# Optimization experiments

Hardware: AMD Instinct MI355X
Metric: run time of the kernel (lower is better)

## Reference

```python
import math
import jax, jax.numpy as jnp
import numpy as np

D_MODEL = 1024
NHEAD = 16
HEAD_DIM = D_MODEL // NHEAD
BATCH = 2
SEQ = 2048


def setup_inputs() -> dict:
    key = jax.random.key(0)
    ks = jax.random.split(key, 8)
    data = jax.random.normal(ks[0], (BATCH, SEQ, D_MODEL), dtype=jnp.float32)
    temporal = jax.random.uniform(ks[1], (BATCH, SEQ), dtype=jnp.float32)
    mask = jnp.zeros((SEQ, SEQ), dtype=jnp.float32)
    s = 1.0 / math.sqrt(D_MODEL)
    Wq = jax.random.normal(ks[2], (D_MODEL, D_MODEL), dtype=jnp.float32) * s
    Wk = jax.random.normal(ks[3], (D_MODEL, D_MODEL), dtype=jnp.float32) * s
    Wv = jax.random.normal(ks[4], (D_MODEL, D_MODEL), dtype=jnp.float32) * s
    bq = jax.random.normal(ks[5], (D_MODEL,), dtype=jnp.float32) * 0.02
    bk = jax.random.normal(ks[6], (D_MODEL,), dtype=jnp.float32) * 0.02
    bv = jax.random.normal(ks[7], (D_MODEL,), dtype=jnp.float32) * 0.02
    return {"data": data, "temporal": temporal, "mask": mask,
            "Wq": Wq, "bq": bq, "Wk": Wk, "bk": bk, "Wv": Wv, "bv": bv}


def _rotate_half_pairs(x):
    # x: [..., s] with s even; pairs (x0,x1) -> (-x1, x0) interleaved
    x2 = x.reshape(x.shape[:-1] + (-1, 2))  # [..., s//2, 2]
    rot = jnp.stack([-x2[..., 1], x2[..., 0]], axis=-1)
    return rot.reshape(x.shape)


def reference(data, temporal, mask, Wq, bq, Wk, bk, Wv, bv):
    B, L, D = data.shape
    H, S = NHEAD, HEAD_DIM
    scale = math.sqrt(S)

    query = (data @ Wq + bq).reshape(B, L, H, S)
    key_ = (data @ Wk + bk).reshape(B, L, H, S)
    value = (data @ Wv + bv).reshape(B, L, H, S)

    # freq = 10000^(-arange(0, S, 2)/S), repeat_interleave(2) -> [S]
    freq = jnp.power(10000.0, -jnp.arange(0, S, 2, dtype=jnp.float32) / S)
    freq = jnp.repeat(freq, 2)
    freqs = temporal[:, :, None] * freq[None, None, :]  # [B, L, S]
    cosine = jnp.cos(freqs)[:, :, None, :]  # [B, L, 1, S]
    sine = jnp.sin(freqs)[:, :, None, :]

    rq = query * cosine + _rotate_half_pairs(query) * sine
    rk = key_ * cosine + _rotate_half_pairs(key_) * sine

    logits = jnp.einsum('bqhs,bkhs->bhqk', rq, rk) / scale
    logits = logits + mask  # mask: [L, L], broadcasts over b,h
    weights = jax.nn.softmax(logits, axis=-1)
    context = jnp.einsum('bhqk,bkhs->bqhs', weights, value)
    return context.reshape(B, L, D)
```

## Files before the change

kernel.cpp:

```cpp
#include <hip/hip_runtime.h>
#include <hip/hip_bf16.h>

#define D_MODEL 1024
#define NHEAD   16
#define HEAD_DIM 64
#define BATCH   2
#define SEQ     2048
#define NTOK    (BATCH*SEQ)

#define FREQ_LOG2 0.20762050593046015f

typedef short  bfrag __attribute__((ext_vector_type(8)));
typedef float  ffrag __attribute__((ext_vector_type(4)));

__device__ inline ushort f2bf(float x) {
    __hip_bfloat16 h = __float2bfloat16(x);
    return __builtin_bit_cast(ushort, h);
}
__device__ inline float bf2f(ushort u) {
    return __builtin_bit_cast(float, (uint)u << 16);
}
__device__ inline void split_bf(float x, ushort& hi, ushort& lo) {
    __hip_bfloat16 h = __float2bfloat16(x);
    hi = __builtin_bit_cast(ushort, h);
    lo = f2bf(x - __bfloat162float(h));
}

__device__ inline void gload16(const ushort* g, ushort* l) {
    __builtin_amdgcn_global_load_lds(
        (const __attribute__((address_space(1))) void*)g,
        (__attribute__((address_space(3))) void*)l, 16, 0, 0);
}

__device__ inline void barrier_lds_only() {
    asm volatile("s_waitcnt lgkmcnt(0)\n\ts_barrier" ::: "memory");
}

__global__ __launch_bounds__(256)
void prep(const float* __restrict__ data, ushort* __restrict__ Ahi,
          ushort* __restrict__ Alo,
          const float* __restrict__ mask, ushort* __restrict__ Mbf,
          int* __restrict__ MZnz,
          const float* __restrict__ Wq, const float* __restrict__ Wk,
          const float* __restrict__ Wv, ushort* __restrict__ WThi)
{
    __shared__ float T[64][65];
    __shared__ int bnz;
    const int bid = blockIdx.x, t = threadIdx.x;

    if (bid < 4096) {
        const int i4 = (bid * 256 + t) * 4;
        const float4 v = *(const float4*)(data + i4);
        ushort4 h, l;
        split_bf(v.x, h.x, l.x); split_bf(v.y, h.y, l.y);
        split_bf(v.z, h.z, l.z); split_bf(v.w, h.w, l.w);
        *(ushort4*)(Ahi + i4) = h;
        *(ushort4*)(Alo + i4) = l;
        return;
    }
    if (bid < 8192) {
        const int mi = bid - 4096;
        const int i4 = (mi * 256 + t) * 4;
        const float4 v = *(const float4*)(mask + i4);
        ushort4 h;
        h.x = f2bf(v.x); h.y = f2bf(v.y); h.z = f2bf(v.z); h.w = f2bf(v.w);
        *(ushort4*)(Mbf + i4) = h;
        const int nz = (v.x != 0.f) || (v.y != 0.f) || (v.z != 0.f) || (v.w != 0.f);
        if (t == 0) bnz = 0;
        __syncthreads();
        if (nz) atomicOr(&bnz, 1);
        __syncthreads();
        if (t == 0) MZnz[mi] = bnz;
        return;
    }
    const int id  = bid - 8192;
    const int z   = id >> 8;
    const int rem = id & 255;
    const int k0  = (rem & 15) * 64, n0 = (rem >> 4) * 64;
    const float* W = (z == 0) ? Wq : (z == 1) ? Wk : Wv;
    ushort* thi = WThi + (size_t)z * D_MODEL * D_MODEL;

    #pragma unroll
    for (int i = 0; i < 4; i++) {
        const int f = i * 256 + t, r = f >> 4, c = (f & 15) * 4;
        const float4 v = *(const float4*)(W + (size_t)(k0 + r) * D_MODEL + n0 + c);
        T[r][c] = v.x; T[r][c + 1] = v.y; T[r][c + 2] = v.z; T[r][c + 3] = v.w;
    }
    __syncthreads();
    #pragma unroll
    for (int i = 0; i < 4; i++) {
        const int f = i * 256 + t, nr = f >> 4, kc = (f & 15) * 4;
        ushort4 h;
        h.x = f2bf(T[kc + 0][nr]);
        h.y = f2bf(T[kc + 1][nr]);
        h.z = f2bf(T[kc + 2][nr]);
        h.w = f2bf(T[kc + 3][nr]);
        const size_t o = (size_t)(n0 + nr) * D_MODEL + k0 + kc;
        *(ushort4*)(thi + o) = h;
    }
}

#define BK 32

union GemmSM {
    ushort st[2][3][128 * BK];
    float  c[64 * 132];
};

__global__ __launch_bounds__(256, 3)
void gemm_qkv(const ushort* __restrict__ Ahi, const ushort* __restrict__ Alo,
              const ushort* __restrict__ WThi,
              const float* __restrict__ bq, const float* __restrict__ bk,
              const float* __restrict__ bv, const float* __restrict__ temporal,
              const int* __restrict__ MZnz, int* __restrict__ Flag,
              ushort* __restrict__ Qhi, ushort* __restrict__ Qlo,
              ushort* __restrict__ Khi,
              ushort* __restrict__ VT)
{
    __shared__ GemmSM sm;
    __shared__ int flg;
    const int bidl = blockIdx.x;
    const int xcd  = bidl & 7, kk = bidl >> 3;
    const int m0   = (xcd * 4 + (kk & 3)) * 128;
    const int nz   = kk >> 2;
    const int n0   = (nz & 7) * 128;
    const int z    = nz >> 3;

    const int t = threadIdx.x;

    if (bidl == 0) {
        if (t == 0) flg = 0;
        __syncthreads();
        int acc = 0;
        const int4* z4 = (const int4*)MZnz;
        #pragma unroll
        for (int i = 0; i < 4; i++) {
            const int4 v = z4[t * 4 + i];
            acc |= v.x | v.y | v.z | v.w;
        }
        if (acc) atomicOr(&flg, 1);
        __syncthreads();
        if (t == 0) Flag[0] = flg;
    }

    const float* bias = (z == 0) ? bq : (z == 1) ? bk : bv;
    const ushort* Bh = WThi + (size_t)z * D_MODEL * D_MODEL;

    const int w = t >> 6, lane = t & 63;
    const int lane15 = lane & 15, quad8 = (lane >> 4) * 8, quad = lane >> 4;
    const int wm = (w >> 1) * 64, wn = (w & 1) * 64;

    ffrag acc[4][4];
    #pragma unroll
    for (int i = 0; i < 4; i++)
        #pragma unroll
        for (int j = 0; j < 4; j++) acc[i][j] = (ffrag){0.f, 0.f, 0.f, 0.f};

    const int wr = w * 32;
    const int lr = lane >> 2;
    const int lc = (((lane & 3) ^ ((lane >> 3) & 3))) * 8;

    auto stage = [&](int bsel, int k0) {
        #pragma unroll
        for (int ch = 0; ch < 2; ch++) {
            const int rb = wr + ch * 16;
            const ushort* ga = Ahi + (size_t)(m0 + rb + lr) * D_MODEL + k0 + lc;
            const ushort* gl = Alo + (size_t)(m0 + rb + lr) * D_MODEL + k0 + lc;
            const ushort* gb = Bh  + (size_t)(n0 + rb + lr) * D_MODEL + k0 + lc;
            gload16(ga, &sm.st[bsel][0][rb * BK]);
            gload16(gl, &sm.st[bsel][1][rb * BK]);
            gload16(gb, &sm.st[bsel][2][rb * BK]);
        }
    };

    stage(0, 0);
    __syncthreads();

    const int rdsw = (quad ^ ((lane15 >> 1) & 3)) * 8;

    int buf = 0;
    for (int k0 = 0; k0 < D_MODEL; k0 += BK) {
        if (k0 + BK < D_MODEL) stage(buf ^ 1, k0 + BK);

        bfrag ah[4], al[4];
        #pragma unroll
        for (int mt = 0; mt < 4; mt++) {
            ah[mt] = *(const bfrag*)&sm.st[buf][0][(wm + mt * 16 + lane15) * BK + rdsw];
            al[mt] = *(const bfrag*)&sm.st[buf][1][(wm + mt * 16 + lane15) * BK + rdsw];
        }
        #pragma unroll
        for (int nt = 0; nt < 4; nt++) {
            const bfrag bh = *(const bfrag*)&sm.st[buf][2][(wn + nt * 16 + lane15) * BK + rdsw];
            #pragma unroll
            for (int mt = 0; mt < 4; mt++) {
                ffrag a = acc[mt][nt];
                a = __builtin_amdgcn_mfma_f32_16x16x32_bf16(ah[mt], bh, a, 0, 0, 0);
                a = __builtin_amdgcn_mfma_f32_16x16x32_bf16(al[mt], bh, a, 0, 0, 0);
                acc[mt][nt] = a;
            }
        }
        __syncthreads();
        buf ^= 1;
    }

    float bn[4];
    #pragma unroll
    for (int nt = 0; nt < 4; nt++) bn[nt] = bias[n0 + wn + nt * 16 + lane15];

    const int CST = (z == 2) ? 129 : 132;

    #pragma unroll
    for (int p = 0; p < 2; p++) {
        if (p) __syncthreads();
        if ((w >> 1) == p) {
            #pragma unroll
            for (int mt = 0; mt < 4; mt++)
                #pragma unroll
                for (int nt = 0; nt < 4; nt++)
                    #pragma unroll
                    for (int rr = 0; rr < 4; rr++)
                        sm.c[(mt * 16 + quad * 4 + rr) * CST + wn + nt * 16 + lane15] =
                            acc[mt][nt][rr] + bn[nt];
        }
        __syncthreads();

        if (z < 2) {
            ushort* ohi = (z == 0) ? Qhi : Khi;
            const float sc = (z == 0) ? 0.125f : 1.0f;
            #pragma unroll
            for (int i = 0; i < 8; i++) {
                const int f = i * 256 + t, r = f >> 5, c4 = (f & 31) * 4;
                float4 v = *(float4*)&sm.c[r * 132 + c4];
                const int m = m0 + p * 64 + r;
                const float tv = temporal[m];
                const float fr0 = exp2f(-(float)(c4 & 63) * FREQ_LOG2);
                const float fr1 = exp2f(-(float)((c4 + 2) & 63) * FREQ_LOG2);
                float s0, c0, s1, c1v;
                __sincosf(tv * fr0, &s0, &c0);
                __sincosf(tv * fr1, &s1, &c1v);
                const float y0 = (v.x * c0 - v.y * s0) * sc;
                const float y1 = (v.y * c0 + v.x * s0) * sc;
                const float y2 = (v.z * c1v - v.w * s1) * sc;
                const float y3 = (v.w * c1v + v.z * s1) * sc;
                ushort4 h, l;
                split_bf(y0, h.x, l.x); split_bf(y1, h.y, l.y);
                split_bf(y2, h.z, l.z); split_bf(y3, h.w, l.w);
                const size_t o = (size_t)m * D_MODEL + n0 + c4;
                *(ushort4*)(ohi + o) = h;
                if (z == 0) *(ushort4*)(Qlo + o) = l;
            }
        } else {
            const int bb = m0 >> 11;
            #pragma unroll
            for (int i = 0; i < 4; i++) {
                const int cid = i * 256 + t, col = cid >> 3, tg = (cid & 7) * 8;
                ushort u8[8];
                #pragma unroll
                for (int j = 0; j < 8; j++) u8[j] = f2bf(sm.c[(tg + j) * 129 + col]);
                const int ncol = n0 + col, hh = ncol >> 6, d = ncol & 63;
                const size_t dst = ((size_t)(bb * NHEAD + hh) * HEAD_DIM + d) * SEQ +
                                   (m0 & (SEQ - 1)) + p * 64 + tg;
                *(int4*)(VT + dst) = *(int4*)u8;
            }
        }
    }
}

__global__ __launch_bounds__(256, 2)
void attn_mfma(const ushort* __restrict__ Qhi, const ushort* __restrict__ Qlo,
               const ushort* __restrict__ Khi,
               const ushort* __restrict__ VT,  const ushort* __restrict__ maskbf,
               const int* __restrict__ Flag,
               float* __restrict__ out)
{
    __shared__ ushort lsK[2][64 * 64], lsV[2][64 * 64], lsP[128 * 64];

    const int bid  = blockIdx.x;
    const int bh   = (bid & 7) * 4 + (bid >> 7);
    const int qb   = (bid >> 3) & 15;
    const int b    = bh >> 4, h = bh & 15;
    const int q0   = qb * 128;

    const int t = threadIdx.x, w = t >> 6, lane = t & 63;
    const int lane15 = lane & 15, quad = lane >> 4;
    const size_t tok0 = (size_t)b * SEQ;

    const int mz = Flag[0];

    bfrag qh[2][2], ql[2][2];
    #pragma unroll
    for (int su = 0; su < 2; su++) {
        const size_t qrow = (tok0 + q0 + w * 32 + su * 16 + lane15) * D_MODEL +
                            h * HEAD_DIM;
        #pragma unroll
        for (int ks = 0; ks < 2; ks++) {
            qh[su][ks] = *(const bfrag*)(Qhi + qrow + ks * 32 + quad * 8);
            ql[su][ks] = *(const bfrag*)(Qlo + qrow + ks * 32 + quad * 8);
        }
    }

    ffrag of[2][4];
    float l_i[2][4];
    #pragma unroll
    for (int su = 0; su < 2; su++)
        #pragma unroll
        for (int nt = 0; nt < 4; nt++) {
            of[su][nt] = (ffrag){0.f, 0.f, 0.f, 0.f};
            l_i[su][nt] = 0.f;
        }

    const int r1 = t >> 3,  c1 = (t & 7) * 8;
    const int sw = ((t & 7) ^ (r1 & 7)) * 8;
    const ushort* Kh0 = Khi + tok0 * D_MODEL + h * HEAD_DIM;
    const ushort* Vt0 = VT + (size_t)(b * NHEAD + h) * HEAD_DIM * SEQ;

    int4 pk0 = *(const int4*)(Kh0 + (size_t)r1 * D_MODEL + c1);
    int4 pk1 = *(const int4*)(Kh0 + (size_t)(32 + r1) * D_MODEL + c1);
    int4 pv0 = *(const int4*)(Vt0 + (size_t)r1 * SEQ + c1);
    int4 pv1 = *(const int4*)(Vt0 + (size_t)(32 + r1) * SEQ + c1);

    *(int4*)&lsK[0][r1 * 64 + sw]        = pk0;
    *(int4*)&lsK[0][(32 + r1) * 64 + sw] = pk1;
    *(int4*)&lsV[0][r1 * 64 + sw]        = pv0;
    *(int4*)&lsV[0][(32 + r1) * 64 + sw] = pv1;

    pk0 = *(const int4*)(Kh0 + (size_t)(64 + r1) * D_MODEL + c1);
    pk1 = *(const int4*)(Kh0 + (size_t)(96 + r1) * D_MODEL + c1);
    pv0 = *(const int4*)(Vt0 + (size_t)r1 * SEQ + 64 + c1);
    pv1 = *(const int4*)(Vt0 + (size_t)(32 + r1) * SEQ + 64 + c1);
    barrier_lds_only();

    const ushort* mrow0 = maskbf + (size_t)(q0 + w * 32 + quad * 4) * SEQ;
    const ushort* mrow1 = maskbf + (size_t)(q0 + w * 32 + 16 + quad * 4) * SEQ;

    const int krd  = lane15 & 7;
    const int keyr = (((lane15 >> 2) & 3) << 1) | (lane15 & 1);

    int cur = 0;
    for (int kt = 0; kt < SEQ; kt += 64) {
        if (kt + 64 < SEQ) {
            *(int4*)&lsK[cur ^ 1][r1 * 64 + sw]        = pk0;
            *(int4*)&lsK[cur ^ 1][(32 + r1) * 64 + sw] = pk1;
            *(int4*)&lsV[cur ^ 1][r1 * 64 + sw]        = pv0;
            *(int4*)&lsV[cur ^ 1][(32 + r1) * 64 + sw] = pv1;
        }

        float mv0[4][4], mv1[4][4];
        if (mz) {
            #pragma unroll
            for (int nt = 0; nt < 4; nt++)
                #pragma unroll
                for (int rr = 0; rr < 4; rr++) {
                    mv0[nt][rr] = bf2f(mrow0[(size_t)rr * SEQ + kt + nt * 16 + lane15]);
                    mv1[nt][rr] = bf2f(mrow1[(size_t)rr * SEQ + kt + nt * 16 + lane15]);
                }
        }

        const int ktn = (kt + 128 < SEQ) ? kt + 128 : 0;
        pk0 = *(const int4*)(Kh0 + (size_t)(ktn + r1) * D_MODEL + c1);
        pk1 = *(const int4*)(Kh0 + (size_t)(ktn + 32 + r1) * D_MODEL + c1);
        pv0 = *(const int4*)(Vt0 + (size_t)r1 * SEQ + ktn + c1);
        pv1 = *(const int4*)(Vt0 + (size_t)(32 + r1) * SEQ + ktn + c1);

        ffrag s0[4], s1[4];
        __builtin_amdgcn_s_setprio(1);
        #pragma unroll
        for (int nt = 0; nt < 4; nt++) {
            const bfrag kf0 = *(const bfrag*)&lsK[cur][(nt * 16 + lane15) * 64 +
                                                       ((0 + quad) ^ krd) * 8];
            const bfrag kf1 = *(const bfrag*)&lsK[cur][(nt * 16 + lane15) * 64 +
                                                       ((4 + quad) ^ krd) * 8];
            ffrag a0 = (ffrag){0.f, 0.f, 0.f, 0.f};
            ffrag a1 = (ffrag){0.f, 0.f, 0.f, 0.f};
            a0 = __builtin_amdgcn_mfma_f32_16x16x32_bf16(qh[0][0], kf0, a0, 0, 0, 0);
            a0 = __builtin_amdgcn_mfma_f32_16x16x32_bf16(ql[0][0], kf0, a0, 0, 0, 0);
            a0 = __builtin_amdgcn_mfma_f32_16x16x32_bf16(qh[0][1], kf1, a0, 0, 0, 0);
            a0 = __builtin_amdgcn_mfma_f32_16x16x32_bf16(ql[0][1], kf1, a0, 0, 0, 0);
            a1 = __builtin_amdgcn_mfma_f32_16x16x32_bf16(qh[1][0], kf0, a1, 0, 0, 0);
            a1 = __builtin_amdgcn_mfma_f32_16x16x32_bf16(ql[1][0], kf0, a1, 0, 0, 0);
            a1 = __builtin_amdgcn_mfma_f32_16x16x32_bf16(qh[1][1], kf1, a1, 0, 0, 0);
            a1 = __builtin_amdgcn_mfma_f32_16x16x32_bf16(ql[1][1], kf1, a1, 0, 0, 0);
            s0[nt] = a0;
            s1[nt] = a1;
        }
        __builtin_amdgcn_s_setprio(0);

        #pragma unroll
        for (int nt = 0; nt < 4; nt++)
            #pragma unroll
            for (int rr = 0; rr < 4; rr++) {
                const int pchk = (2 * nt + (lane15 >> 3)) ^ ((quad << 1) | (rr & 1));
                float x0 = s0[nt][rr];
                float x1 = s1[nt][rr];
                if (mz) { x0 += mv0[nt][rr]; x1 += mv1[nt][rr]; }
                const float e0 = __expf(x0);
                l_i[0][rr] += e0;
                lsP[(w * 32 + quad * 4 + rr) * 64 + pchk * 8 + (lane15 & 7)] = f2bf(e0);
                const float e1 = __expf(x1);
                l_i[1][rr] += e1;
                lsP[(w * 32 + 16 + quad * 4 + rr) * 64 + pchk * 8 + (lane15 & 7)] = f2bf(e1);
            }

        __builtin_amdgcn_s_setprio(1);
        #pragma unroll
        for (int ks = 0; ks < 2; ks++) {
            const bfrag pf0 = *(const bfrag*)&lsP[(w * 32 + lane15) * 64 +
                                                  ((ks * 4 + quad) ^ keyr) * 8];
            const bfrag pf1 = *(const bfrag*)&lsP[(w * 32 + 16 + lane15) * 64 +
                                                  ((ks * 4 + quad) ^ keyr) * 8];
            #pragma unroll
            for (int nt = 0; nt < 4; nt++) {
                const bfrag vf = *(const bfrag*)&lsV[cur][(nt * 16 + lane15) * 64 +
                                                          ((ks * 4 + quad) ^ krd) * 8];
                of[0][nt] = __builtin_amdgcn_mfma_f32_16x16x32_bf16(pf0, vf, of[0][nt], 0, 0, 0);
                of[1][nt] = __builtin_amdgcn_mfma_f32_16x16x32_bf16(pf1, vf, of[1][nt], 0, 0, 0);
            }
        }
        __builtin_amdgcn_s_setprio(0);

        barrier_lds_only();
        cur ^= 1;
    }

    #pragma unroll
    for (int su = 0; su < 2; su++) {
        float inv[4];
        #pragma unroll
        for (int rr = 0; rr < 4; rr++) {
            float v = l_i[su][rr];
            #pragma unroll
            for (int off = 1; off < 16; off <<= 1) v += __shfl_xor(v, off);
            inv[rr] = 1.0f / v;
        }
        #pragma unroll
        for (int nt = 0; nt < 4; nt++)
            #pragma unroll
            for (int rr = 0; rr < 4; rr++)
                out[(tok0 + q0 + w * 32 + su * 16 + quad * 4 + rr) * D_MODEL +
                    h * HEAD_DIM + nt * 16 + lane15] = of[su][nt][rr] * inv[rr];
    }
}

extern "C" void kernel_launch(void* const* d_in, const int* in_sizes, int n_in,
                              void* d_out, int out_size, void* d_ws, size_t ws_size,
                              hipStream_t stream)
{
    const float* data     = (const float*)d_in[0];
    const float* temporal = (const float*)d_in[1];
    const float* mask     = (const float*)d_in[2];
    const float* Wq = (const float*)d_in[3];
    const float* bq = (const float*)d_in[4];
    const float* Wk = (const float*)d_in[5];
    const float* bk = (const float*)d_in[6];
    const float* Wv = (const float*)d_in[7];
    const float* bv = (const float*)d_in[8];
    float* out = (float*)d_out;

    char* ws = (char*)d_ws;
    const size_t MB = 1024 * 1024;
    ushort* Ahi  = (ushort*)(ws + 0 * MB);
    ushort* Alo  = (ushort*)(ws + 8 * MB);
    ushort* WThi = (ushort*)(ws + 16 * MB);
    int*    MZnz = (int*)   (ws + 22 * MB);
    int*    Flag = (int*)   (ws + 23 * MB);
    ushort* Qhi  = (ushort*)(ws + 28 * MB);
    ushort* Qlo  = (ushort*)(ws + 36 * MB);
    ushort* Khi  = (ushort*)(ws + 44 * MB);
    ushort* VT   = (ushort*)(ws + 60 * MB);
    ushort* Mbf  = (ushort*)(ws + 68 * MB);

    prep<<<dim3(8960), 256, 0, stream>>>(data, Ahi, Alo, mask, Mbf, MZnz,
                                         Wq, Wk, Wv, WThi);
    gemm_qkv<<<dim3(768), 256, 0, stream>>>(
        Ahi, Alo, WThi, bq, bk, bv, temporal, MZnz, Flag,
        Qhi, Qlo, Khi, VT);
    attn_mfma<<<dim3(BATCH * NHEAD * SEQ / 128), 256, 0, stream>>>(
        Qhi, Qlo, Khi, VT, Mbf, Flag, out);
}
```

Baseline: 252.1 us.

## Load A-lo fragments directly to registers, shrink LDS, precompute RoPE cos/sin table

The GEMM stops staging the low-order A split through LDS. Each wave now prefetches its Alo MFMA fragments straight from global memory into registers one K-step ahead, which cuts shared-memory footprint and lets occupancy rise from 3 to 4 blocks per CU. The barrier is relaxed to a partial vmcnt wait so the register prefetch can stay in flight across it. RoPE cos/sin values are precomputed into a table by extra blocks in the prep kernel, so the GEMM epilogue no longer evaluates sincos, at the cost of extra global traffic and register pressure.

Result: no change. 249.4 us (-1.0%).

```diff
diff --git a/kernel.cpp b/kernel.cpp
--- a/kernel.cpp
+++ b/kernel.cpp
@@ -36,13 +36,18 @@
     asm volatile("s_waitcnt lgkmcnt(0)\n\ts_barrier" ::: "memory");
 }
 
+__device__ inline void barrier_vm4() {
+    asm volatile("s_waitcnt vmcnt(4) lgkmcnt(0)\n\ts_barrier" ::: "memory");
+}
+
 __global__ __launch_bounds__(256)
 void prep(const float* __restrict__ data, ushort* __restrict__ Ahi,
           ushort* __restrict__ Alo,
           const float* __restrict__ mask, ushort* __restrict__ Mbf,
           int* __restrict__ MZnz,
           const float* __restrict__ Wq, const float* __restrict__ Wk,
-          const float* __restrict__ Wv, ushort* __restrict__ WThi)
+          const float* __restrict__ Wv, ushort* __restrict__ WThi,
+          const float* __restrict__ temporal, float* __restrict__ cst)
 {
     __shared__ float T[64][65];
     __shared__ int bnz;
@@ -73,45 +78,56 @@
         if (t == 0) MZnz[mi] = bnz;
         return;
     }
-    const int id  = bid - 8192;
-    const int z   = id >> 8;
-    const int rem = id & 255;
-    const int k0  = (rem & 15) * 64, n0 = (rem >> 4) * 64;
-    const float* W = (z == 0) ? Wq : (z == 1) ? Wk : Wv;
-    ushort* thi = WThi + (size_t)z * D_MODEL * D_MODEL;
-
-    #pragma unroll
-    for (int i = 0; i < 4; i++) {
-        const int f = i * 256 + t, r = f >> 4, c = (f & 15) * 4;
-        const float4 v = *(const float4*)(W + (size_t)(k0 + r) * D_MODEL + n0 + c);
-        T[r][c] = v.x; T[r][c + 1] = v.y; T[r][c + 2] = v.z; T[r][c + 3] = v.w;
-    }
-    __syncthreads();
-    #pragma unroll
-    for (int i = 0; i < 4; i++) {
-        const int f = i * 256 + t, nr = f >> 4, kc = (f & 15) * 4;
-        ushort4 h;
-        h.x = f2bf(T[kc + 0][nr]);
-        h.y = f2bf(T[kc + 1][nr]);
-        h.z = f2bf(T[kc + 2][nr]);
-        h.w = f2bf(T[kc + 3][nr]);
-        const size_t o = (size_t)(n0 + nr) * D_MODEL + k0 + kc;
-        *(ushort4*)(thi + o) = h;
-    }
+    if (bid < 8960) {
+        const int id  = bid - 8192;
+        const int z   = id >> 8;
+        const int rem = id & 255;
+        const int k0  = (rem & 15) * 64, n0 = (rem >> 4) * 64;
+        const float* W = (z == 0) ? Wq : (z == 1) ? Wk : Wv;
+        ushort* thi = WThi + (size_t)z * D_MODEL * D_MODEL;
+
+        #pragma unroll
+        for (int i = 0; i < 4; i++) {
+            const int f = i * 256 + t, r = f >> 4, c = (f & 15) * 4;
+            const float4 v = *(const float4*)(W + (size_t)(k0 + r) * D_MODEL + n0 + c);
+            T[r][c] = v.x; T[r][c + 1] = v.y; T[r][c + 2] = v.z; T[r][c + 3] = v.w;
+        }
+        __syncthreads();
+        #pragma unroll
+        for (int i = 0; i < 4; i++) {
+            const int f = i * 256 + t, nr = f >> 4, kc = (f & 15) * 4;
+            ushort4 h;
+            h.x = f2bf(T[kc + 0][nr]);
+            h.y = f2bf(T[kc + 1][nr]);
+            h.z = f2bf(T[kc + 2][nr]);
+            h.w = f2bf(T[kc + 3][nr]);
+            const size_t o = (size_t)(n0 + nr) * D_MODEL + k0 + kc;
+            *(ushort4*)(thi + o) = h;
+        }
+        return;
+    }
+    const int id3 = bid - 8960;
+    const int m   = id3 * 8 + (t >> 5);
+    const int j   = t & 31;
+    const float tv = temporal[m];
+    const float fr = exp2f(-(float)(2 * j) * FREQ_LOG2);
+    float s, c;
+    __sincosf(tv * fr, &s, &c);
+    *(float2*)(cst + (size_t)m * 64 + 2 * j) = make_float2(c, s);
 }
 
 #define BK 32
 
 union GemmSM {
-    ushort st[2][3][128 * BK];
+    ushort st[2][2][128 * BK];
     float  c[64 * 132];
 };
 
-__global__ __launch_bounds__(256, 3)
+__global__ __launch_bounds__(256, 4)
 void gemm_qkv(const ushort* __restrict__ Ahi, const ushort* __restrict__ Alo,
               const ushort* __restrict__ WThi,
               const float* __restrict__ bq, const float* __restrict__ bk,
-              const float* __restrict__ bv, const float* __restrict__ temporal,
+              const float* __restrict__ bv, const float* __restrict__ cst,
               const int* __restrict__ MZnz, int* __restrict__ Flag,
               ushort* __restrict__ Qhi, ushort* __restrict__ Qlo,
               ushort* __restrict__ Khi,
@@ -165,13 +181,24 @@
         for (int ch = 0; ch < 2; ch++) {
             const int rb = wr + ch * 16;
             const ushort* ga = Ahi + (size_t)(m0 + rb + lr) * D_MODEL + k0 + lc;
-            const ushort* gl = Alo + (size_t)(m0 + rb + lr) * D_MODEL + k0 + lc;
             const ushort* gb = Bh  + (size_t)(n0 + rb + lr) * D_MODEL + k0 + lc;
             gload16(ga, &sm.st[bsel][0][rb * BK]);
-            gload16(gl, &sm.st[bsel][1][rb * BK]);
-            gload16(gb, &sm.st[bsel][2][rb * BK]);
+            gload16(gb, &sm.st[bsel][1][rb * BK]);
         }
     };
+
+    const size_t arow[1] = {0};
+    bfrag alp0, alp1, alp2, alp3;
+    {
+        const size_t r0 = (size_t)(m0 + wm +  0 + lane15) * D_MODEL + quad8;
+        const size_t r1_ = (size_t)(m0 + wm + 16 + lane15) * D_MODEL + quad8;
+        const size_t r2 = (size_t)(m0 + wm + 32 + lane15) * D_MODEL + quad8;
+        const size_t r3 = (size_t)(m0 + wm + 48 + lane15) * D_MODEL + quad8;
+        alp0 = *(const bfrag*)(Alo + r0);
+        alp1 = *(const bfrag*)(Alo + r1_);
+        alp2 = *(const bfrag*)(Alo + r2);
+        alp3 = *(const bfrag*)(Alo + r3);
+    }
 
     stage(0, 0);
     __syncthreads();
@@ -182,24 +209,49 @@
     for (int k0 = 0; k0 < D_MODEL; k0 += BK) {
         if (k0 + BK < D_MODEL) stage(buf ^ 1, k0 + BK);
 
-        bfrag ah[4], al[4];
-        #pragma unroll
-        for (int mt = 0; mt < 4; mt++) {
+        bfrag al0 = alp0, al1 = alp1, al2 = alp2, al3 = alp3;
+        if (k0 + BK < D_MODEL) {
+            const int kn = k0 + BK;
+            alp0 = *(const bfrag*)(Alo + (size_t)(m0 + wm +  0 + lane15) * D_MODEL + kn + quad8);
+            alp1 = *(const bfrag*)(Alo + (size_t)(m0 + wm + 16 + lane15) * D_MODEL + kn + quad8);
+            alp2 = *(const bfrag*)(Alo + (size_t)(m0 + wm + 32 + lane15) * D_MODEL + kn + quad8);
+            alp3 = *(const bfrag*)(Alo + (size_t)(m0 + wm + 48 + lane15) * D_MODEL + kn + quad8);
+        }
+
+        bfrag ah[4];
+        #pragma unroll
+        for (int mt = 0; mt < 4; mt++)
             ah[mt] = *(const bfrag*)&sm.st[buf][0][(wm + mt * 16 + lane15) * BK + rdsw];
-            al[mt] = *(const bfrag*)&sm.st[buf][1][(wm + mt * 16 + lane15) * BK + rdsw];
-        }
+
         #pragma unroll
         for (int nt = 0; nt < 4; nt++) {
-            const bfrag bh = *(const bfrag*)&sm.st[buf][2][(wn + nt * 16 + lane15) * BK + rdsw];
-            #pragma unroll
-            for (int mt = 0; mt < 4; mt++) {
-                ffrag a = acc[mt][nt];
-                a = __builtin_amdgcn_mfma_f32_16x16x32_bf16(ah[mt], bh, a, 0, 0, 0);
-                a = __builtin_amdgcn_mfma_f32_16x16x32_bf16(al[mt], bh, a, 0, 0, 0);
-                acc[mt][nt] = a;
-            }
-        }
-        __syncthreads();
+            const bfrag bh = *(const bfrag*)&sm.st[buf][1][(wn + nt * 16 + lane15) * BK + rdsw];
+            {
+                ffrag a = acc[0][nt];
+                a = __builtin_amdgcn_mfma_f32_16x16x32_bf16(ah[0], bh, a, 0, 0, 0);
+                a = __builtin_amdgcn_mfma_f32_16x16x32_bf16(al0,   bh, a, 0, 0, 0);
+                acc[0][nt] = a;
+            }
+            {
+                ffrag a = acc[1][nt];
+                a = __builtin_amdgcn_mfma_f32_16x16x32_bf16(ah[1], bh, a, 0, 0, 0);
+                a = __builtin_amdgcn_mfma_f32_16x16x32_bf16(al1,   bh, a, 0, 0, 0);
+                acc[1][nt] = a;
+            }
+            {
+                ffrag a = acc[2][nt];
+                a = __builtin_amdgcn_mfma_f32_16x16x32_bf16(ah[2], bh, a, 0, 0, 0);
+                a = __builtin_amdgcn_mfma_f32_16x16x32_bf16(al2,   bh, a, 0, 0, 0);
+                acc[2][nt] = a;
+            }
+            {
+                ffrag a = acc[3][nt];
+                a = __builtin_amdgcn_mfma_f32_16x16x32_bf16(ah[3], bh, a, 0, 0, 0);
+                a = __builtin_amdgcn_mfma_f32_16x16x32_bf16(al3,   bh, a, 0, 0, 0);
+                acc[3][nt] = a;
+            }
+        }
+        barrier_vm4();
         buf ^= 1;
     }
 
@@ -232,12 +284,8 @@
                 const int f = i * 256 + t, r = f >> 5, c4 = (f & 31) * 4;
                 float4 v = *(float4*)&sm.c[r * 132 + c4];
                 const int m = m0 + p * 64 + r;
-                const float tv = temporal[m];
-                const float fr0 = exp2f(-(float)(c4 & 63) * FREQ_LOG2);
-                const float fr1 = exp2f(-(float)((c4 + 2) & 63) * FREQ_LOG2);
-                float s0, c0, s1, c1v;
-                __sincosf(tv * fr0, &s0, &c0);
-                __sincosf(tv * fr1, &s1, &c1v);
+                const float4 cs4 = *(const float4*)(cst + (size_t)m * 64 + (c4 & 63));
+                const float c0 = cs4.x, s0 = cs4.y, c1v = cs4.z, s1 = cs4.w;
                 const float y0 = (v.x * c0 - v.y * s0) * sc;
                 const float y1 = (v.y * c0 + v.x * s0) * sc;
                 const float y2 = (v.z * c1v - v.w * s1) * sc;
@@ -463,16 +511,17 @@
     ushort* WThi = (ushort*)(ws + 16 * MB);
     int*    MZnz = (int*)   (ws + 22 * MB);
     int*    Flag = (int*)   (ws + 23 * MB);
+    float*  cst  = (float*) (ws + 24 * MB);
     ushort* Qhi  = (ushort*)(ws + 28 * MB);
     ushort* Qlo  = (ushort*)(ws + 36 * MB);
     ushort* Khi  = (ushort*)(ws + 44 * MB);
     ushort* VT   = (ushort*)(ws + 60 * MB);
     ushort* Mbf  = (ushort*)(ws + 68 * MB);
 
-    prep<<<dim3(8960), 256, 0, stream>>>(data, Ahi, Alo, mask, Mbf, MZnz,
-                                         Wq, Wk, Wv, WThi);
+    prep<<<dim3(9472), 256, 0, stream>>>(data, Ahi, Alo, mask, Mbf, MZnz,
+                                         Wq, Wk, Wv, WThi, temporal, cst);
     gemm_qkv<<<dim3(768), 256, 0, stream>>>(
-        Ahi, Alo, WThi, bq, bk, bv, temporal, MZnz, Flag,
+        Ahi, Alo, WThi, bq, bk, bv, cst, MZnz, Flag,
         Qhi, Qlo, Khi, VT);
     attn_mfma<<<dim3(BATCH * NHEAD * SEQ / 128), 256, 0, stream>>>(
         Qhi, Qlo, Khi, VT, Mbf, Flag, out);
```
